# Optimization experiments

Measured on AMD Instinct MI355X. Metric: run time of the kernel, lower is better.

Reference implementation:

```python
import jax, jax.numpy as jnp
import numpy as np
from jax import lax

IMG_DIM = 512
D_MODEL = 768
N_LAYER = 12
D_INNER = 2 * D_MODEL          # 1536
D_STATE = 16
D_CONV = 4
DT_RANK = (D_MODEL + 15) // 16 # 48
BATCH = 4
SEQ = 256


def setup_inputs() -> dict:
    key = jax.random.key(0)
    ks = jax.random.split(key, 16)
    s = 0.02
    inp = {
        "frames_rep": jax.random.normal(ks[0], (BATCH, SEQ, IMG_DIM), jnp.float32),
        "fproj_w": jax.random.normal(ks[1], (IMG_DIM, D_MODEL), jnp.float32) * s,
        "fproj_b": jnp.zeros((D_MODEL,), jnp.float32),
        "norm_w": jnp.ones((N_LAYER, D_MODEL), jnp.float32),
        "in_w": jax.random.normal(ks[2], (N_LAYER, D_MODEL, 2 * D_INNER), jnp.float32) * s,
        "conv_w": jax.random.normal(ks[3], (N_LAYER, D_INNER, D_CONV), jnp.float32) * s,
        "conv_b": jnp.zeros((N_LAYER, D_INNER), jnp.float32),
        "xproj_w": jax.random.normal(ks[4], (N_LAYER, D_INNER, DT_RANK + 2 * D_STATE), jnp.float32) * s,
        "dt_w": jax.random.normal(ks[5], (N_LAYER, DT_RANK, D_INNER), jnp.float32) * s,
        "dt_b": jnp.full((N_LAYER, D_INNER), -2.0, jnp.float32),  # softplus(-2)~0.13
        "A_log": jnp.broadcast_to(jnp.log(jnp.arange(1, D_STATE + 1, dtype=jnp.float32)), (N_LAYER, D_INNER, D_STATE)) * jnp.ones((N_LAYER, D_INNER, 1)),
        "D_param": jnp.ones((N_LAYER, D_INNER), jnp.float32),
        "out_w": jax.random.normal(ks[6], (N_LAYER, D_INNER, D_MODEL), jnp.float32) * s,
        "normf_w": jnp.ones((D_MODEL,), jnp.float32),
    }
    return inp


def _rmsnorm(x, w, eps=1e-5):
    return x * lax.rsqrt(jnp.mean(x * x, axis=-1, keepdims=True) + eps) * w


def _mamba_layer(x, in_w, conv_w, conv_b, xproj_w, dt_w, dt_b, A_log, D_param, out_w):
    # x: (B, L, D_MODEL)
    B, L, _ = x.shape
    xz = x @ in_w                                  # (B, L, 2*di)
    xi, res = jnp.split(xz, 2, axis=-1)            # each (B, L, di)
    # depthwise causal conv over time
    xc = jnp.transpose(xi, (0, 2, 1))              # (B, di, L)
    xc = lax.conv_general_dilated(
        xc, conv_w[:, None, :], (1,), [(D_CONV - 1, 0)],
        feature_group_count=D_INNER)
    xi = jax.nn.silu(jnp.transpose(xc + conv_b[None, :, None], (0, 2, 1)))
    # input-dependent SSM parameters
    x_dbl = xi @ xproj_w                           # (B, L, dt_rank + 2n)
    delta = x_dbl[..., :DT_RANK]
    Bm = x_dbl[..., DT_RANK:DT_RANK + D_STATE]     # (B, L, n)
    Cm = x_dbl[..., DT_RANK + D_STATE:]            # (B, L, n)
    delta = jax.nn.softplus(delta @ dt_w + dt_b)   # (B, L, di)
    A = -jnp.exp(A_log)                            # (di, n)
    deltaA = jnp.exp(delta[..., None] * A)                               # (B, L, di, n)
    deltaBu = delta[..., None] * Bm[:, :, None, :] * xi[..., None]       # (B, L, di, n)

    def step(h, inp):
        dA, dBu, c = inp
        h = dA * h + dBu                           # (B, di, n)
        y = jnp.einsum('bdn,bn->bd', h, c)
        return h, y

    xs = (deltaA.transpose(1, 0, 2, 3), deltaBu.transpose(1, 0, 2, 3), Cm.transpose(1, 0, 2))
    h0 = jnp.zeros((B, D_INNER, D_STATE), x.dtype)
    _, ys = lax.scan(step, h0, xs)                 # (L, B, di)
    y = ys.transpose(1, 0, 2) + xi * D_param
    y = y * jax.nn.silu(res)
    return y @ out_w                               # (B, L, D_MODEL)


def reference(frames_rep, fproj_w, fproj_b, norm_w, in_w, conv_w, conv_b,
              xproj_w, dt_w, dt_b, A_log, D_param, out_w, normf_w):
    h = jax.nn.relu(frames_rep @ fproj_w + fproj_b)       # (B, L, D_MODEL)
    for i in range(N_LAYER):
        h = h + _mamba_layer(_rmsnorm(h, norm_w[i]), in_w[i], conv_w[i], conv_b[i],
                             xproj_w[i], dt_w[i], dt_b[i], A_log[i], D_param[i], out_w[i])
    return _rmsnorm(h, normf_w)
```

## Files before the change

### kernel.cpp

```cpp
#include <hip/hip_runtime.h>
#include <hip/hip_bf16.h>
#include <cmath>

#define IMG_DIM 512
#define D_MODEL 768
#define N_LAYER 12
#define D_INNER 1536
#define D_STATE 16
#define D_CONV 4
#define DT_RANK 48
#define BATCH 4
#define SEQ 256
#define M_TOK (BATCH * SEQ)
#define XPROJ_N (DT_RANK + 2 * D_STATE)
#define KSPLIT 8
#define NCHUNK 16
#define CLEN 16
#define LOG2E 1.4426950408889634f

typedef __attribute__((ext_vector_type(8))) short bf16x8;
typedef __attribute__((ext_vector_type(4))) float f32x4;

__device__ __forceinline__ float softplus_f(float v) {
    return v > 20.f ? v : log1pf(expf(v));
}

__global__ __launch_bounds__(256) void wcvt_t_k(
    const float* __restrict__ W, __hip_bfloat16* __restrict__ WT,
    int K, int N)
{
    __shared__ float tile[32][33];
    const int tx = threadIdx.x & 31;
    const int ty4 = (threadIdx.x >> 5) * 4;
    const int n0 = blockIdx.x * 32, k0 = blockIdx.y * 32;
    #pragma unroll
    for (int r = 0; r < 4; ++r)
        tile[ty4 + r][tx] = (n0 + tx < N)
            ? W[(size_t)(k0 + ty4 + r) * N + n0 + tx] : 0.f;
    __syncthreads();
    #pragma unroll
    for (int r = 0; r < 4; ++r)
        if (n0 + ty4 + r < N)
            WT[(size_t)(n0 + ty4 + r) * K + k0 + tx] =
                __float2bfloat16(tile[tx][ty4 + r]);
}

__global__ __launch_bounds__(256) void cvt_bf16_k(
    const float* __restrict__ in, __hip_bfloat16* __restrict__ out, int n)
{
    int i = blockIdx.x * 256 + threadIdx.x;
    if (i < n) out[i] = __float2bfloat16(in[i]);
}

__global__ __launch_bounds__(256) void dtw_cvt_k(
    const float* __restrict__ dt_w, __hip_bfloat16* __restrict__ dtwT)
{
    int idx = blockIdx.x * 256 + threadIdx.x;
    int k = idx & 63, n = idx >> 6;
    dtwT[idx] = (k < DT_RANK)
        ? __float2bfloat16(dt_w[(size_t)k * D_INNER + n])
        : __hip_bfloat16(0.f);
}

__global__ __launch_bounds__(256) void a2_k(
    const float* __restrict__ A_log, float* __restrict__ A2)
{
    int idx = blockIdx.x * 256 + threadIdx.x;
    A2[idx] = -expf(A_log[idx]) * LOG2E;
}

template <int EPI>
__global__ __launch_bounds__(256) void gemm_bf16(
    const __hip_bfloat16* __restrict__ A,
    const __hip_bfloat16* __restrict__ BT,
    float* __restrict__ C, int ldc, int K,
    const float* __restrict__ bias)
{
    __shared__ __align__(16) char lds[2][16384];
    const int tid = threadIdx.x;
    const int lane = tid & 63;
    const int wid = tid >> 6;
    const int wr = wid >> 1, wc = wid & 1;
    const size_t rowBase = blockIdx.x * 64;
    const size_t colBase = blockIdx.y * 64;

    const int r0 = tid >> 3;
    const int cb0 = (tid & 7) * 16;
    const int wOffA = r0 * 128 + (cb0 ^ ((r0 & 7) << 4));
    const char* gA = (const char*)(A + rowBase * K);
    const char* gB = (const char*)(BT + colBase * K);
    const size_t rowByteOff = (size_t)r0 * K * 2 + cb0;

    const int lrow = lane & 15;
    const int kg = (lane >> 4) * 16;
    const int swz = (lane & 7) << 4;

    f32x4 acc[2][2] = {};

    const int nt = K >> 6;
    float4 ra0, ra1, rb0, rb1;

    ra0 = *(const float4*)(gA + rowByteOff);
    ra1 = *(const float4*)(gA + rowByteOff + (size_t)32 * K * 2);
    rb0 = *(const float4*)(gB + rowByteOff);
    rb1 = *(const float4*)(gB + rowByteOff + (size_t)32 * K * 2);
    *(float4*)(&lds[0][wOffA])        = ra0;
    *(float4*)(&lds[0][wOffA + 4096]) = ra1;
    *(float4*)(&lds[0][wOffA + 8192]) = rb0;
    *(float4*)(&lds[0][wOffA + 12288])= rb1;
    __syncthreads();

    for (int t = 0; t < nt; ++t) {
        const int cur = t & 1;
        if (t + 1 < nt) {
            size_t off = rowByteOff + (size_t)(t + 1) * 128;
            ra0 = *(const float4*)(gA + off);
            ra1 = *(const float4*)(gA + off + (size_t)32 * K * 2);
            rb0 = *(const float4*)(gB + off);
            rb1 = *(const float4*)(gB + off + (size_t)32 * K * 2);
        }
        #pragma unroll
        for (int kk = 0; kk < 2; ++kk) {
            const int col = (kk * 64 + kg) ^ swz;
            bf16x8 a0 = *(const bf16x8*)(&lds[cur][(wr * 32 +      lrow) * 128 + col]);
            bf16x8 a1 = *(const bf16x8*)(&lds[cur][(wr * 32 + 16 + lrow) * 128 + col]);
            bf16x8 b0 = *(const bf16x8*)(&lds[cur][8192 + (wc * 32 +      lrow) * 128 + col]);
            bf16x8 b1 = *(const bf16x8*)(&lds[cur][8192 + (wc * 32 + 16 + lrow) * 128 + col]);
            acc[0][0] = __builtin_amdgcn_mfma_f32_16x16x32_bf16(a0, b0, acc[0][0], 0, 0, 0);
            acc[0][1] = __builtin_amdgcn_mfma_f32_16x16x32_bf16(a0, b1, acc[0][1], 0, 0, 0);
            acc[1][0] = __builtin_amdgcn_mfma_f32_16x16x32_bf16(a1, b0, acc[1][0], 0, 0, 0);
            acc[1][1] = __builtin_amdgcn_mfma_f32_16x16x32_bf16(a1, b1, acc[1][1], 0, 0, 0);
        }
        if (t + 1 < nt) {
            const int nxt = cur ^ 1;
            *(float4*)(&lds[nxt][wOffA])        = ra0;
            *(float4*)(&lds[nxt][wOffA + 4096]) = ra1;
            *(float4*)(&lds[nxt][wOffA + 8192]) = rb0;
            *(float4*)(&lds[nxt][wOffA + 12288])= rb1;
        }
        __syncthreads();
    }

    const int mBase = (int)rowBase + wr * 32 + (lane >> 4) * 4;
    const int nBase = (int)colBase + wc * 32 + (lane & 15);
    #pragma unroll
    for (int i = 0; i < 2; ++i)
        #pragma unroll
        for (int j = 0; j < 2; ++j)
            #pragma unroll
            for (int rg = 0; rg < 4; ++rg) {
                int cc = nBase + j * 16;
                size_t idx = (size_t)(mBase + i * 16 + rg) * ldc + cc;
                float v = acc[i][j][rg];
                if (EPI == 0) {
                    C[idx] = v;
                } else if (EPI == 1) {
                    v += bias[cc];
                    C[idx] = v > 0.f ? v : 0.f;
                } else if (EPI == 2) {
                    v += bias[cc];
                    C[idx] = softplus_f(v);
                } else {
                    C[idx] += v;
                }
            }
}

__global__ __launch_bounds__(256) void xproj_gemm_k(
    const __hip_bfloat16* __restrict__ xc_bf,
    const __hip_bfloat16* __restrict__ xprojT,
    float* __restrict__ part)
{
    const int lane = threadIdx.x & 63;
    const int w = threadIdx.x >> 6;
    const int m0 = blockIdx.x * 64 + w * 16;
    const int ks = blockIdx.y;
    const int KS = D_INNER / KSPLIT;
    const int k0 = ks * KS;

    const int arow = m0 + (lane & 15);
    const int kgrp = (lane >> 4) * 8;

    f32x4 acc[5] = {};
    const __hip_bfloat16* ap = xc_bf + (size_t)arow * D_INNER + kgrp;
    const __hip_bfloat16* bp = xprojT + (size_t)(lane & 15) * D_INNER + kgrp;

    for (int k = k0; k < k0 + KS; k += 32) {
        bf16x8 a = *(const bf16x8*)(ap + k);
        #pragma unroll
        for (int f = 0; f < 5; ++f) {
            bf16x8 b = *(const bf16x8*)(bp + (size_t)f * 16 * D_INNER + k);
            acc[f] = __builtin_amdgcn_mfma_f32_16x16x32_bf16(a, b, acc[f], 0, 0, 0);
        }
    }

    float* out = part + (size_t)ks * M_TOK * XPROJ_N;
    const int rowb = blockIdx.x * 64 + w * 16 + (lane >> 4) * 4;
    #pragma unroll
    for (int f = 0; f < 5; ++f)
        #pragma unroll
        for (int rg = 0; rg < 4; ++rg)
            out[(size_t)(rowb + rg) * XPROJ_N + f * 16 + (lane & 15)] = acc[f][rg];
}

__global__ __launch_bounds__(256) void xproj_reduce_k(
    const float* __restrict__ part, float* __restrict__ xdbl,
    __hip_bfloat16* __restrict__ dtin)
{
    int idx = blockIdx.x * 256 + threadIdx.x;
    float s = 0.f;
    #pragma unroll
    for (int p = 0; p < KSPLIT; ++p)
        s += part[(size_t)p * M_TOK * XPROJ_N + idx];
    xdbl[idx] = s;
    int col = idx % XPROJ_N;
    int row = idx / XPROJ_N;
    if (col < DT_RANK)
        dtin[(size_t)row * 64 + col] = __float2bfloat16(s);
}

template <typename OT>
__global__ __launch_bounds__(256) void rmsnorm_k(
    const float* __restrict__ x, const float* __restrict__ w,
    OT* __restrict__ o)
{
    const int row = blockIdx.x;
    const float* xr = x + (size_t)row * D_MODEL;
    float v[3];
    float s = 0.f;
    #pragma unroll
    for (int i = 0; i < 3; ++i) {
        v[i] = xr[threadIdx.x + i * 256];
        s = fmaf(v[i], v[i], s);
    }
    #pragma unroll
    for (int off = 32; off > 0; off >>= 1) s += __shfl_down(s, off);
    __shared__ float red[4];
    if ((threadIdx.x & 63) == 0) red[threadIdx.x >> 6] = s;
    __syncthreads();
    float tot = red[0] + red[1] + red[2] + red[3];
    float r = rsqrtf(tot * (1.f / D_MODEL) + 1e-5f);
    OT* orow = o + (size_t)row * D_MODEL;
    #pragma unroll
    for (int i = 0; i < 3; ++i) {
        int c = threadIdx.x + i * 256;
        orow[c] = (OT)(v[i] * r * w[c]);
    }
}

__global__ __launch_bounds__(256) void conv_silu_k(
    const float* __restrict__ xz, const float* __restrict__ cw,
    const float* __restrict__ cb, float* __restrict__ xc,
    __hip_bfloat16* __restrict__ xc_bf)
{
    int idx = blockIdx.x * 256 + threadIdx.x;
    int d = idx % D_INNER;
    int bt = idx / D_INNER;
    int t = bt & (SEQ - 1);
    int b = bt >> 8;
    float acc = cb[d];
    #pragma unroll
    for (int k = 0; k < 4; ++k) {
        int tt = t - 3 + k;
        if (tt >= 0)
            acc = fmaf(xz[(size_t)(b * SEQ + tt) * (2 * D_INNER) + d], cw[d * 4 + k], acc);
    }
    float sig = 1.f / (1.f + expf(-acc));
    float v = acc * sig;
    xc[idx] = v;
    xc_bf[idx] = __float2bfloat16(v);
}

__global__ __launch_bounds__(256) void scan_part_k(
    const float* __restrict__ delta,
    const float* __restrict__ xc,
    const float* __restrict__ xdbl,
    const float* __restrict__ A2,
    const float* __restrict__ D_param,
    float* __restrict__ cumdv,
    float* __restrict__ ypart,
    float* __restrict__ hpart)
{
    __shared__ float sBC[CLEN][32];
    const int tid = threadIdx.x;
    const int dgrp  = blockIdx.x % 6;
    const int chunk = (blockIdx.x / 6) & (NCHUNK - 1);
    const int b     = blockIdx.x / (6 * NCHUNK);
    const int d  = dgrp * 256 + tid;
    const int t0 = chunk * CLEN;

    {
        int r = tid >> 5, c = tid & 31;
        sBC[r][c]     = xdbl[(size_t)(b * SEQ + t0 + r) * XPROJ_N + DT_RANK + c];
        sBC[r + 8][c] = xdbl[(size_t)(b * SEQ + t0 + r + 8) * XPROJ_N + DT_RANK + c];
    }

    float a2[16];
    {
        const float4* ap = (const float4*)(A2 + (size_t)d * 16);
        #pragma unroll
        for (int q = 0; q < 4; ++q) {
            float4 v = ap[q];
            a2[q * 4 + 0] = v.x; a2[q * 4 + 1] = v.y;
            a2[q * 4 + 2] = v.z; a2[q * 4 + 3] = v.w;
        }
    }
    const float Dp = D_param[d];

    const size_t base = (size_t)(b * SEQ + t0) * D_INNER + d;
    const float* dp = delta + base;
    const float* up = xc + base;

    float dvv[CLEN], uvv[CLEN];
    #pragma unroll
    for (int s = 0; s < CLEN; ++s) {
        dvv[s] = dp[(size_t)s * D_INNER];
        uvv[s] = up[(size_t)s * D_INNER];
    }
    __syncthreads();

    float h[16];
    #pragma unroll
    for (int n = 0; n < 16; ++n) h[n] = 0.f;
    float cum = 0.f;

    #pragma unroll
    for (int s = 0; s < CLEN; ++s) {
        float dv = dvv[s], u = uvv[s];
        cum += dv;
        cumdv[base + (size_t)s * D_INNER] = cum;
        float du = dv * u;
        float yv = 0.f;
        #pragma unroll
        for (int n = 0; n < 16; ++n) {
            float dA = exp2f(dv * a2[n]);
            h[n] = fmaf(dA, h[n], du * sBC[s][n]);
            yv = fmaf(h[n], sBC[s][16 + n], yv);
        }
        ypart[base + (size_t)s * D_INNER] = fmaf(u, Dp, yv);
    }

    float4* hp = (float4*)(hpart + (((size_t)b * NCHUNK + chunk) * D_INNER + d) * 16);
    #pragma unroll
    for (int q = 0; q < 4; ++q) {
        float4 v;
        v.x = h[q * 4 + 0]; v.y = h[q * 4 + 1];
        v.z = h[q * 4 + 2]; v.w = h[q * 4 + 3];
        hp[q] = v;
    }
}

__global__ __launch_bounds__(256) void scan_pref_k(
    const float* __restrict__ cumdv,
    const float* __restrict__ hpart,
    const float* __restrict__ A2,
    float* __restrict__ hinb)
{
    int idx = blockIdx.x * 256 + threadIdx.x;
    int n = idx & 15;
    int r = idx >> 4;
    int d = r % D_INNER;
    int b = r / D_INNER;
    float a2 = A2[(size_t)d * 16 + n];
    float hin = 0.f;
    #pragma unroll
    for (int c = 0; c < NCHUNK; ++c) {
        hinb[(((size_t)b * NCHUNK + c) * D_INNER + d) * 16 + n] = hin;
        float sdv = cumdv[(size_t)(b * SEQ + c * CLEN + CLEN - 1) * D_INNER + d];
        float hp  = hpart[(((size_t)b * NCHUNK + c) * D_INNER + d) * 16 + n];
        hin = fmaf(hin, exp2f(a2 * sdv), hp);
    }
}

__global__ __launch_bounds__(256) void scan_fix_k(
    const float* __restrict__ ypart,
    const float* __restrict__ cumdv,
    const float* __restrict__ xdbl,
    const float* __restrict__ xz,
    const float* __restrict__ A2,
    const float* __restrict__ hinb,
    __hip_bfloat16* __restrict__ y)
{
    __shared__ float sC[16];
    int idx = blockIdx.x * 256 + threadIdx.x;
    int d = idx % D_INNER;
    int bt = idx / D_INNER;
    int t = bt & (SEQ - 1);
    int b = bt >> 8;
    int chunk = t >> 4;

    if (threadIdx.x < 16)
        sC[threadIdx.x] = xdbl[(size_t)bt * XPROJ_N + DT_RANK + D_STATE + threadIdx.x];
    __syncthreads();

    float cum = cumdv[idx];
    float yp  = ypart[idx];
    float res = xz[(size_t)bt * 2 * D_INNER + D_INNER + d];

    const float4* hp = (const float4*)(hinb + (((size_t)b * NCHUNK + chunk) * D_INNER + d) * 16);
    const float4* ap = (const float4*)(A2 + (size_t)d * 16);

    float corr = 0.f;
    #pragma unroll
    for (int q = 0; q < 4; ++q) {
        float4 hv = hp[q];
        float4 av = ap[q];
        corr = fmaf(exp2f(av.x * cum) * hv.x, sC[q * 4 + 0], corr);
        corr = fmaf(exp2f(av.y * cum) * hv.y, sC[q * 4 + 1], corr);
        corr = fmaf(exp2f(av.z * cum) * hv.z, sC[q * 4 + 2], corr);
        corr = fmaf(exp2f(av.w * cum) * hv.w, sC[q * 4 + 3], corr);
    }
    float sr = res / (1.f + expf(-res));
    y[idx] = __float2bfloat16((yp + corr) * sr);
}

extern "C" void kernel_launch(void* const* d_in, const int* in_sizes, int n_in,
                              void* d_out, int out_size, void* d_ws, size_t ws_size,
                              hipStream_t stream)
{
    const float* frames  = (const float*)d_in[0];
    const float* fproj_w = (const float*)d_in[1];
    const float* fproj_b = (const float*)d_in[2];
    const float* norm_w  = (const float*)d_in[3];
    const float* in_w    = (const float*)d_in[4];
    const float* conv_w  = (const float*)d_in[5];
    const float* conv_b  = (const float*)d_in[6];
    const float* xproj_w = (const float*)d_in[7];
    const float* dt_w    = (const float*)d_in[8];
    const float* dt_b    = (const float*)d_in[9];
    const float* A_log   = (const float*)d_in[10];
    const float* D_param = (const float*)d_in[11];
    const float* out_w   = (const float*)d_in[12];
    const float* normf_w = (const float*)d_in[13];

    char* ws = (char*)d_ws;
    float* h      = (float*)ws;                   ws += (size_t)M_TOK * D_MODEL * 4;
    float* xz     = (float*)ws;                   ws += (size_t)M_TOK * 2 * D_INNER * 4;
    float* xc     = (float*)ws;                   ws += (size_t)M_TOK * D_INNER * 4;
    float* xdbl   = (float*)ws;                   ws += (size_t)M_TOK * XPROJ_N * 4;
    float* delta  = (float*)ws;                   ws += (size_t)M_TOK * D_INNER * 4;
    float* part   = (float*)ws;                   ws += (size_t)KSPLIT * M_TOK * XPROJ_N * 4;
    float* A2b    = (float*)ws;                   ws += (size_t)D_INNER * 16 * 4;
    float* cumdv  = (float*)ws;                   ws += (size_t)M_TOK * D_INNER * 4;
    float* ypartb = (float*)ws;                   ws += (size_t)M_TOK * D_INNER * 4;
    float* hpartb = (float*)ws;                   ws += (size_t)BATCH * NCHUNK * D_INNER * 16 * 4;
    float* hinb   = (float*)ws;                   ws += (size_t)BATCH * NCHUNK * D_INNER * 16 * 4;
    __hip_bfloat16* x_bf   = (__hip_bfloat16*)ws; ws += (size_t)M_TOK * D_MODEL * 2;
    __hip_bfloat16* y_bf   = (__hip_bfloat16*)ws; ws += (size_t)M_TOK * D_INNER * 2;
    __hip_bfloat16* xc_bf  = (__hip_bfloat16*)ws; ws += (size_t)M_TOK * D_INNER * 2;
    __hip_bfloat16* dtin   = (__hip_bfloat16*)ws; ws += (size_t)M_TOK * 64 * 2;
    __hip_bfloat16* fr_bf  = (__hip_bfloat16*)ws; ws += (size_t)M_TOK * IMG_DIM * 2;
    __hip_bfloat16* fp_wT  = (__hip_bfloat16*)ws; ws += (size_t)D_MODEL * IMG_DIM * 2;
    __hip_bfloat16* in_wT  = (__hip_bfloat16*)ws; ws += (size_t)(2 * D_INNER) * D_MODEL * 2;
    __hip_bfloat16* out_wT = (__hip_bfloat16*)ws; ws += (size_t)D_MODEL * D_INNER * 2;
    __hip_bfloat16* xprojT = (__hip_bfloat16*)ws; ws += (size_t)XPROJ_N * D_INNER * 2;
    __hip_bfloat16* dt_wT  = (__hip_bfloat16*)ws; ws += (size_t)D_INNER * 64 * 2;

    dim3 blk(256);

    hipMemsetAsync(dtin, 0, (size_t)M_TOK * 64 * 2, stream);

    cvt_bf16_k<<<(M_TOK * IMG_DIM) / 256, blk, 0, stream>>>(
        frames, fr_bf, M_TOK * IMG_DIM);
    wcvt_t_k<<<dim3(D_MODEL / 32, IMG_DIM / 32), blk, 0, stream>>>(
        fproj_w, fp_wT, IMG_DIM, D_MODEL);
    gemm_bf16<1><<<dim3(M_TOK / 64, D_MODEL / 64), blk, 0, stream>>>(
        fr_bf, fp_wT, h, D_MODEL, IMG_DIM, fproj_b);

    for (int i = 0; i < N_LAYER; ++i) {
        const float* in_wi    = in_w    + (size_t)i * D_MODEL * 2 * D_INNER;
        const float* conv_wi  = conv_w  + (size_t)i * D_INNER * D_CONV;
        const float* conv_bi  = conv_b  + (size_t)i * D_INNER;
        const float* xproj_wi = xproj_w + (size_t)i * D_INNER * XPROJ_N;
        const float* dt_wi    = dt_w    + (size_t)i * DT_RANK * D_INNER;
        const float* dt_bi    = dt_b    + (size_t)i * D_INNER;
        const float* A_logi   = A_log   + (size_t)i * D_INNER * D_STATE;
        const float* D_parami = D_param + (size_t)i * D_INNER;
        const float* out_wi   = out_w   + (size_t)i * D_INNER * D_MODEL;
        const float* norm_wi  = norm_w  + (size_t)i * D_MODEL;

        rmsnorm_k<__hip_bfloat16><<<M_TOK, blk, 0, stream>>>(h, norm_wi, x_bf);
        wcvt_t_k<<<dim3(2 * D_INNER / 32, D_MODEL / 32), blk, 0, stream>>>(
            in_wi, in_wT, D_MODEL, 2 * D_INNER);
        gemm_bf16<0><<<dim3(M_TOK / 64, (2 * D_INNER) / 64), blk, 0, stream>>>(
            x_bf, in_wT, xz, 2 * D_INNER, D_MODEL, nullptr);
        conv_silu_k<<<(M_TOK * D_INNER) / 256, blk, 0, stream>>>(
            xz, conv_wi, conv_bi, xc, xc_bf);
        wcvt_t_k<<<dim3((XPROJ_N + 31) / 32, D_INNER / 32), blk, 0, stream>>>(
            xproj_wi, xprojT, D_INNER, XPROJ_N);
        xproj_gemm_k<<<dim3(M_TOK / 64, KSPLIT), blk, 0, stream>>>(
            xc_bf, xprojT, part);
        xproj_reduce_k<<<(M_TOK * XPROJ_N) / 256, blk, 0, stream>>>(
            part, xdbl, dtin);
        dtw_cvt_k<<<(D_INNER * 64) / 256, blk, 0, stream>>>(dt_wi, dt_wT);
        gemm_bf16<2><<<dim3(M_TOK / 64, D_INNER / 64), blk, 0, stream>>>(
            dtin, dt_wT, delta, D_INNER, 64, dt_bi);
        a2_k<<<(D_INNER * 16) / 256, blk, 0, stream>>>(A_logi, A2b);
        scan_part_k<<<BATCH * NCHUNK * (D_INNER / 256), blk, 0, stream>>>(
            delta, xc, xdbl, A2b, D_parami, cumdv, ypartb, hpartb);
        scan_pref_k<<<(BATCH * D_INNER * 16) / 256, blk, 0, stream>>>(
            cumdv, hpartb, A2b, hinb);
        scan_fix_k<<<(M_TOK * D_INNER) / 256, blk, 0, stream>>>(
            ypartb, cumdv, xdbl, xz, A2b, hinb, y_bf);
        wcvt_t_k<<<dim3(D_MODEL / 32, D_INNER / 32), blk, 0, stream>>>(
            out_wi, out_wT, D_INNER, D_MODEL);
        gemm_bf16<3><<<dim3(M_TOK / 64, D_MODEL / 64), blk, 0, stream>>>(
            y_bf, out_wT, h, D_MODEL, D_INNER, nullptr);
    }

    rmsnorm_k<float><<<M_TOK, blk, 0, stream>>>(h, normf_w, (float*)d_out);
}
```

Baseline: 1.424 ms.

## Batch all-layer weight conversion upfront and store intermediates in bf16

All per-layer weight transposes and bf16 conversions (in_w, out_w, xproj_w, dt_w, A2) now run once before the layer loop as batched launches over a z-dimension, which removes about 60 small kernel launches. The xz, delta and conv-output activations are stored in bf16 instead of fp32, so the fp32 xc copy goes away and traffic through conv, scan and fix roughly halves. In exchange the workspace grows to hold every layer's converted weights, and storing delta and the gate in bf16 lowers precision.

```diff
diff --git a/kernel.cpp b/kernel.cpp
--- a/kernel.cpp
+++ b/kernel.cpp
@@ -20,16 +20,19 @@
 
 typedef __attribute__((ext_vector_type(8))) short bf16x8;
 typedef __attribute__((ext_vector_type(4))) float f32x4;
+typedef __hip_bfloat16 bf16;
 
 __device__ __forceinline__ float softplus_f(float v) {
     return v > 20.f ? v : log1pf(expf(v));
 }
+__device__ __forceinline__ float b2f(bf16 v) { return __bfloat162float(v); }
 
 __global__ __launch_bounds__(256) void wcvt_t_k(
-    const float* __restrict__ W, __hip_bfloat16* __restrict__ WT,
-    int K, int N)
+    const float* __restrict__ W, bf16* __restrict__ WT, int K, int N)
 {
     __shared__ float tile[32][33];
+    W  += (size_t)blockIdx.z * K * N;
+    WT += (size_t)blockIdx.z * K * N;
     const int tx = threadIdx.x & 31;
     const int ty4 = (threadIdx.x >> 5) * 4;
     const int n0 = blockIdx.x * 32, k0 = blockIdx.y * 32;
@@ -46,20 +49,22 @@
 }
 
 __global__ __launch_bounds__(256) void cvt_bf16_k(
-    const float* __restrict__ in, __hip_bfloat16* __restrict__ out, int n)
+    const float* __restrict__ in, bf16* __restrict__ out, int n)
 {
     int i = blockIdx.x * 256 + threadIdx.x;
     if (i < n) out[i] = __float2bfloat16(in[i]);
 }
 
 __global__ __launch_bounds__(256) void dtw_cvt_k(
-    const float* __restrict__ dt_w, __hip_bfloat16* __restrict__ dtwT)
+    const float* __restrict__ dt_w, bf16* __restrict__ dtwT)
 {
     int idx = blockIdx.x * 256 + threadIdx.x;
-    int k = idx & 63, n = idx >> 6;
+    int k = idx & 63;
+    int n = (idx >> 6) % D_INNER;
+    int l = idx / (64 * D_INNER);
     dtwT[idx] = (k < DT_RANK)
-        ? __float2bfloat16(dt_w[(size_t)k * D_INNER + n])
-        : __hip_bfloat16(0.f);
+        ? __float2bfloat16(dt_w[((size_t)l * DT_RANK + k) * D_INNER + n])
+        : bf16(0.f);
 }
 
 __global__ __launch_bounds__(256) void a2_k(
@@ -69,11 +74,11 @@
     A2[idx] = -expf(A_log[idx]) * LOG2E;
 }
 
-template <int EPI>
+template <int EPI, typename OT>
 __global__ __launch_bounds__(256) void gemm_bf16(
-    const __hip_bfloat16* __restrict__ A,
-    const __hip_bfloat16* __restrict__ BT,
-    float* __restrict__ C, int ldc, int K,
+    const bf16* __restrict__ A,
+    const bf16* __restrict__ BT,
+    OT* __restrict__ C, int ldc, int K,
     const float* __restrict__ bias)
 {
     __shared__ __align__(16) char lds[2][16384];
@@ -153,13 +158,13 @@
                 size_t idx = (size_t)(mBase + i * 16 + rg) * ldc + cc;
                 float v = acc[i][j][rg];
                 if (EPI == 0) {
-                    C[idx] = v;
+                    C[idx] = (OT)v;
                 } else if (EPI == 1) {
                     v += bias[cc];
-                    C[idx] = v > 0.f ? v : 0.f;
+                    C[idx] = (OT)(v > 0.f ? v : 0.f);
                 } else if (EPI == 2) {
                     v += bias[cc];
-                    C[idx] = softplus_f(v);
+                    C[idx] = (OT)softplus_f(v);
                 } else {
                     C[idx] += v;
                 }
@@ -167,8 +172,8 @@
 }
 
 __global__ __launch_bounds__(256) void xproj_gemm_k(
-    const __hip_bfloat16* __restrict__ xc_bf,
-    const __hip_bfloat16* __restrict__ xprojT,
+    const bf16* __restrict__ xc_bf,
+    const bf16* __restrict__ xprojT,
     float* __restrict__ part)
 {
     const int lane = threadIdx.x & 63;
@@ -182,8 +187,8 @@
     const int kgrp = (lane >> 4) * 8;
 
     f32x4 acc[5] = {};
-    const __hip_bfloat16* ap = xc_bf + (size_t)arow * D_INNER + kgrp;
-    const __hip_bfloat16* bp = xprojT + (size_t)(lane & 15) * D_INNER + kgrp;
+    const bf16* ap = xc_bf + (size_t)arow * D_INNER + kgrp;
+    const bf16* bp = xprojT + (size_t)(lane & 15) * D_INNER + kgrp;
 
     for (int k = k0; k < k0 + KS; k += 32) {
         bf16x8 a = *(const bf16x8*)(ap + k);
@@ -205,7 +210,7 @@
 
 __global__ __launch_bounds__(256) void xproj_reduce_k(
     const float* __restrict__ part, float* __restrict__ xdbl,
-    __hip_bfloat16* __restrict__ dtin)
+    bf16* __restrict__ dtin)
 {
     int idx = blockIdx.x * 256 + threadIdx.x;
     float s = 0.f;
@@ -249,9 +254,8 @@
 }
 
 __global__ __launch_bounds__(256) void conv_silu_k(
-    const float* __restrict__ xz, const float* __restrict__ cw,
-    const float* __restrict__ cb, float* __restrict__ xc,
-    __hip_bfloat16* __restrict__ xc_bf)
+    const bf16* __restrict__ xz, const float* __restrict__ cw,
+    const float* __restrict__ cb, bf16* __restrict__ xc_bf)
 {
     int idx = blockIdx.x * 256 + threadIdx.x;
     int d = idx % D_INNER;
@@ -263,17 +267,16 @@
     for (int k = 0; k < 4; ++k) {
         int tt = t - 3 + k;
         if (tt >= 0)
-            acc = fmaf(xz[(size_t)(b * SEQ + tt) * (2 * D_INNER) + d], cw[d * 4 + k], acc);
+            acc = fmaf(b2f(xz[(size_t)(b * SEQ + tt) * (2 * D_INNER) + d]),
+                       cw[d * 4 + k], acc);
     }
     float sig = 1.f / (1.f + expf(-acc));
-    float v = acc * sig;
-    xc[idx] = v;
-    xc_bf[idx] = __float2bfloat16(v);
+    xc_bf[idx] = __float2bfloat16(acc * sig);
 }
 
 __global__ __launch_bounds__(256) void scan_part_k(
-    const float* __restrict__ delta,
-    const float* __restrict__ xc,
+    const bf16* __restrict__ delta,
+    const bf16* __restrict__ xc,
     const float* __restrict__ xdbl,
     const float* __restrict__ A2,
     const float* __restrict__ D_param,
@@ -308,14 +311,14 @@
     const float Dp = D_param[d];
 
     const size_t base = (size_t)(b * SEQ + t0) * D_INNER + d;
-    const float* dp = delta + base;
-    const float* up = xc + base;
+    const bf16* dp = delta + base;
+    const bf16* up = xc + base;
 
     float dvv[CLEN], uvv[CLEN];
     #pragma unroll
     for (int s = 0; s < CLEN; ++s) {
-        dvv[s] = dp[(size_t)s * D_INNER];
-        uvv[s] = up[(size_t)s * D_INNER];
+        dvv[s] = b2f(dp[(size_t)s * D_INNER]);
+        uvv[s] = b2f(up[(size_t)s * D_INNER]);
     }
     __syncthreads();
 
@@ -376,10 +379,10 @@
     const float* __restrict__ ypart,
     const float* __restrict__ cumdv,
     const float* __restrict__ xdbl,
-    const float* __restrict__ xz,
+    const bf16* __restrict__ xz,
     const float* __restrict__ A2,
     const float* __restrict__ hinb,
-    __hip_bfloat16* __restrict__ y)
+    bf16* __restrict__ y)
 {
     __shared__ float sC[16];
     int idx = blockIdx.x * 256 + threadIdx.x;
@@ -395,7 +398,7 @@
 
     float cum = cumdv[idx];
     float yp  = ypart[idx];
-    float res = xz[(size_t)bt * 2 * D_INNER + D_INNER + d];
+    float res = b2f(xz[(size_t)bt * 2 * D_INNER + D_INNER + d]);
 
     const float4* hp = (const float4*)(hinb + (((size_t)b * NCHUNK + chunk) * D_INNER + d) * 16);
     const float4* ap = (const float4*)(A2 + (size_t)d * 16);
@@ -434,78 +437,77 @@
     const float* normf_w = (const float*)d_in[13];
 
     char* ws = (char*)d_ws;
-    float* h      = (float*)ws;                   ws += (size_t)M_TOK * D_MODEL * 4;
-    float* xz     = (float*)ws;                   ws += (size_t)M_TOK * 2 * D_INNER * 4;
-    float* xc     = (float*)ws;                   ws += (size_t)M_TOK * D_INNER * 4;
-    float* xdbl   = (float*)ws;                   ws += (size_t)M_TOK * XPROJ_N * 4;
-    float* delta  = (float*)ws;                   ws += (size_t)M_TOK * D_INNER * 4;
-    float* part   = (float*)ws;                   ws += (size_t)KSPLIT * M_TOK * XPROJ_N * 4;
-    float* A2b    = (float*)ws;                   ws += (size_t)D_INNER * 16 * 4;
-    float* cumdv  = (float*)ws;                   ws += (size_t)M_TOK * D_INNER * 4;
-    float* ypartb = (float*)ws;                   ws += (size_t)M_TOK * D_INNER * 4;
-    float* hpartb = (float*)ws;                   ws += (size_t)BATCH * NCHUNK * D_INNER * 16 * 4;
-    float* hinb   = (float*)ws;                   ws += (size_t)BATCH * NCHUNK * D_INNER * 16 * 4;
-    __hip_bfloat16* x_bf   = (__hip_bfloat16*)ws; ws += (size_t)M_TOK * D_MODEL * 2;
-    __hip_bfloat16* y_bf   = (__hip_bfloat16*)ws; ws += (size_t)M_TOK * D_INNER * 2;
-    __hip_bfloat16* xc_bf  = (__hip_bfloat16*)ws; ws += (size_t)M_TOK * D_INNER * 2;
-    __hip_bfloat16* dtin   = (__hip_bfloat16*)ws; ws += (size_t)M_TOK * 64 * 2;
-    __hip_bfloat16* fr_bf  = (__hip_bfloat16*)ws; ws += (size_t)M_TOK * IMG_DIM * 2;
-    __hip_bfloat16* fp_wT  = (__hip_bfloat16*)ws; ws += (size_t)D_MODEL * IMG_DIM * 2;
-    __hip_bfloat16* in_wT  = (__hip_bfloat16*)ws; ws += (size_t)(2 * D_INNER) * D_MODEL * 2;
-    __hip_bfloat16* out_wT = (__hip_bfloat16*)ws; ws += (size_t)D_MODEL * D_INNER * 2;
-    __hip_bfloat16* xprojT = (__hip_bfloat16*)ws; ws += (size_t)XPROJ_N * D_INNER * 2;
-    __hip_bfloat16* dt_wT  = (__hip_bfloat16*)ws; ws += (size_t)D_INNER * 64 * 2;
+    float* h      = (float*)ws;        ws += (size_t)M_TOK * D_MODEL * 4;
+    float* xdbl   = (float*)ws;        ws += (size_t)M_TOK * XPROJ_N * 4;
+    float* part   = (float*)ws;        ws += (size_t)KSPLIT * M_TOK * XPROJ_N * 4;
+    float* cumdv  = (float*)ws;        ws += (size_t)M_TOK * D_INNER * 4;
+    float* ypartb = (float*)ws;        ws += (size_t)M_TOK * D_INNER * 4;
+    float* hpartb = (float*)ws;        ws += (size_t)BATCH * NCHUNK * D_INNER * 16 * 4;
+    float* hinb   = (float*)ws;        ws += (size_t)BATCH * NCHUNK * D_INNER * 16 * 4;
+    float* A2all  = (float*)ws;        ws += (size_t)N_LAYER * D_INNER * 16 * 4;
+    bf16* xz_bf   = (bf16*)ws;         ws += (size_t)M_TOK * 2 * D_INNER * 2;
+    bf16* xc_bf   = (bf16*)ws;         ws += (size_t)M_TOK * D_INNER * 2;
+    bf16* delta_bf= (bf16*)ws;         ws += (size_t)M_TOK * D_INNER * 2;
+    bf16* x_bf    = (bf16*)ws;         ws += (size_t)M_TOK * D_MODEL * 2;
+    bf16* y_bf    = (bf16*)ws;         ws += (size_t)M_TOK * D_INNER * 2;
+    bf16* dtin    = (bf16*)ws;         ws += (size_t)M_TOK * 64 * 2;
+    bf16* fr_bf   = (bf16*)ws;         ws += (size_t)M_TOK * IMG_DIM * 2;
+    bf16* fp_wT   = (bf16*)ws;         ws += (size_t)D_MODEL * IMG_DIM * 2;
+    bf16* in_wT   = (bf16*)ws;         ws += (size_t)N_LAYER * 2 * D_INNER * D_MODEL * 2;
+    bf16* out_wT  = (bf16*)ws;         ws += (size_t)N_LAYER * D_MODEL * D_INNER * 2;
+    bf16* xprojT  = (bf16*)ws;         ws += (size_t)N_LAYER * XPROJ_N * D_INNER * 2;
+    bf16* dt_wT   = (bf16*)ws;         ws += (size_t)N_LAYER * D_INNER * 64 * 2;
 
     dim3 blk(256);
 
     hipMemsetAsync(dtin, 0, (size_t)M_TOK * 64 * 2, stream);
-
     cvt_bf16_k<<<(M_TOK * IMG_DIM) / 256, blk, 0, stream>>>(
         frames, fr_bf, M_TOK * IMG_DIM);
-    wcvt_t_k<<<dim3(D_MODEL / 32, IMG_DIM / 32), blk, 0, stream>>>(
+    wcvt_t_k<<<dim3(D_MODEL / 32, IMG_DIM / 32, 1), blk, 0, stream>>>(
         fproj_w, fp_wT, IMG_DIM, D_MODEL);
-    gemm_bf16<1><<<dim3(M_TOK / 64, D_MODEL / 64), blk, 0, stream>>>(
+    wcvt_t_k<<<dim3(2 * D_INNER / 32, D_MODEL / 32, N_LAYER), blk, 0, stream>>>(
+        in_w, in_wT, D_MODEL, 2 * D_INNER);
+    wcvt_t_k<<<dim3(D_MODEL / 32, D_INNER / 32, N_LAYER), blk, 0, stream>>>(
+        out_w, out_wT, D_INNER, D_MODEL);
+    wcvt_t_k<<<dim3((XPROJ_N + 31) / 32, D_INNER / 32, N_LAYER), blk, 0, stream>>>(
+        xproj_w, xprojT, D_INNER, XPROJ_N);
+    dtw_cvt_k<<<(N_LAYER * D_INNER * 64) / 256, blk, 0, stream>>>(dt_w, dt_wT);
+    a2_k<<<(N_LAYER * D_INNER * 16) / 256, blk, 0, stream>>>(A_log, A2all);
+
+    gemm_bf16<1, float><<<dim3(M_TOK / 64, D_MODEL / 64), blk, 0, stream>>>(
         fr_bf, fp_wT, h, D_MODEL, IMG_DIM, fproj_b);
 
     for (int i = 0; i < N_LAYER; ++i) {
-        const float* in_wi    = in_w    + (size_t)i * D_MODEL * 2 * D_INNER;
-        const float* conv_wi  = conv_w  + (size_t)i * D_INNER * D_CONV;
-        const float* conv_bi  = conv_b  + (size_t)i * D_INNER;
-        const float* xproj_wi = xproj_w + (size_t)i * D_INNER * XPROJ_N;
-        const float* dt_wi    = dt_w    + (size_t)i * DT_RANK * D_INNER;
-        const float* dt_bi    = dt_b    + (size_t)i * D_INNER;
-        const float* A_logi   = A_log   + (size_t)i * D_INNER * D_STATE;
-        const float* D_parami = D_param + (size_t)i * D_INNER;
-        const float* out_wi   = out_w   + (size_t)i * D_INNER * D_MODEL;
-        const float* norm_wi  = norm_w  + (size_t)i * D_MODEL;
-
-        rmsnorm_k<__hip_bfloat16><<<M_TOK, blk, 0, stream>>>(h, norm_wi, x_bf);
-        wcvt_t_k<<<dim3(2 * D_INNER / 32, D_MODEL / 32), blk, 0, stream>>>(
-            in_wi, in_wT, D_MODEL, 2 * D_INNER);
-        gemm_bf16<0><<<dim3(M_TOK / 64, (2 * D_INNER) / 64), blk, 0, stream>>>(
-            x_bf, in_wT, xz, 2 * D_INNER, D_MODEL, nullptr);
+        const bf16* in_wTi   = in_wT  + (size_t)i * 2 * D_INNER * D_MODEL;
+        const bf16* out_wTi  = out_wT + (size_t)i * D_MODEL * D_INNER;
+        const bf16* xprojTi  = xprojT + (size_t)i * XPROJ_N * D_INNER;
+        const bf16* dt_wTi   = dt_wT  + (size_t)i * D_INNER * 64;
+        const float* A2i     = A2all  + (size_t)i * D_INNER * 16;
+        const float* conv_wi = conv_w + (size_t)i * D_INNER * D_CONV;
+        const float* conv_bi = conv_b + (size_t)i * D_INNER;
+        const float* dt_bi   = dt_b   + (size_t)i * D_INNER;
+        const float* D_parami= D_param+ (size_t)i * D_INNER;
+        const float* norm_wi = norm_w + (size_t)i * D_MODEL;
+
+        rmsnorm_k<bf16><<<M_TOK, blk, 0, stream>>>(h, norm_wi, x_bf);
+        gemm_bf16<0, bf16><<<dim3(M_TOK / 64, (2 * D_INNER) / 64), blk, 0, stream>>>(
+            x_bf, in_wTi, xz_bf, 2 * D_INNER, D_MODEL, nullptr);
         conv_silu_k<<<(M_TOK * D_INNER) / 256, blk, 0, stream>>>(
-            xz, conv_wi, conv_bi, xc, xc_bf);
-        wcvt_t_k<<<dim3((XPROJ_N + 31) / 32, D_INNER / 32), blk, 0, stream>>>(
-            xproj_wi, xprojT, D_INNER, XPROJ_N);
+            xz_bf, conv_wi, conv_bi, xc_bf);
         xproj_gemm_k<<<dim3(M_TOK / 64, KSPLIT), blk, 0, stream>>>(
-            xc_bf, xprojT, part);
+            xc_bf, xprojTi, part);
         xproj_reduce_k<<<(M_TOK * XPROJ_N) / 256, blk, 0, stream>>>(
             part, xdbl, dtin);
-        dtw_cvt_k<<<(D_INNER * 64) / 256, blk, 0, stream>>>(dt_wi, dt_wT);
-        gemm_bf16<2><<<dim3(M_TOK / 64, D_INNER / 64), blk, 0, stream>>>(
-            dtin, dt_wT, delta, D_INNER, 64, dt_bi);
-        a2_k<<<(D_INNER * 16) / 256, blk, 0, stream>>>(A_logi, A2b);
+        gemm_bf16<2, bf16><<<dim3(M_TOK / 64, D_INNER / 64), blk, 0, stream>>>(
+            dtin, dt_wTi, delta_bf, D_INNER, 64, dt_bi);
         scan_part_k<<<BATCH * NCHUNK * (D_INNER / 256), blk, 0, stream>>>(
-            delta, xc, xdbl, A2b, D_parami, cumdv, ypartb, hpartb);
+            delta_bf, xc_bf, xdbl, A2i, D_parami, cumdv, ypartb, hpartb);
         scan_pref_k<<<(BATCH * D_INNER * 16) / 256, blk, 0, stream>>>(
-            cumdv, hpartb, A2b, hinb);
+            cumdv, hpartb, A2i, hinb);
         scan_fix_k<<<(M_TOK * D_INNER) / 256, blk, 0, stream>>>(
-            ypartb, cumdv, xdbl, xz, A2b, hinb, y_bf);
-        wcvt_t_k<<<dim3(D_MODEL / 32, D_INNER / 32), blk, 0, stream>>>(
-            out_wi, out_wT, D_INNER, D_MODEL);
-        gemm_bf16<3><<<dim3(M_TOK / 64, D_MODEL / 64), blk, 0, stream>>>(
-            y_bf, out_wT, h, D_MODEL, D_INNER, nullptr);
+            ypartb, cumdv, xdbl, xz_bf, A2i, hinb, y_bf);
+        gemm_bf16<3, float><<<dim3(M_TOK / 64, D_MODEL / 64), blk, 0, stream>>>(
+            y_bf, out_wTi, h, D_MODEL, D_INNER, nullptr);
     }
 
     rmsnorm_k<float><<<M_TOK, blk, 0, stream>>>(h, normf_w, (float*)d_out);
```

Measured after the change: 1.307 ms. 8.2% less time.
